# Performance work log

Measured on AMD Instinct MI355X. Metric: run time of the kernel, lower is better.

Reference implementation:

```python
import jax, jax.numpy as jnp
import numpy as np

V, E, H, B, L_ENC, T = 32000, 512, 512, 32, 512, 64


def setup_inputs() -> dict:
    key = jax.random.key(0)
    ks = jax.random.split(key, 15)
    s = 0.05  # weight scale to keep activations in a sane range
    return {
        "x": jax.random.randint(ks[0], (B, 1), 0, V),
        "encod_out": jax.random.normal(ks[1], (B, L_ENC, H), jnp.float32),
        "h": jax.random.normal(ks[2], (1, B, H), jnp.float32) * s,
        "c": jax.random.normal(ks[3], (1, B, H), jnp.float32) * s,
        "targets": jax.random.randint(ks[4], (B, T), 0, V),
        "mask_att": jax.random.randint(ks[5], (B, L_ENC), 0, 2).astype(jnp.int32),
        "teacher_forcing_ratio": 1,
        "embed_table": jax.random.normal(ks[6], (V, E), jnp.float32) * s,
        "W_ih": jax.random.normal(ks[7], (4 * H, E + H), jnp.float32) * s,
        "W_hh": jax.random.normal(ks[8], (4 * H, H), jnp.float32) * s,
        "b_ih": jax.random.normal(ks[9], (4 * H,), jnp.float32) * s,
        "b_hh": jax.random.normal(ks[10], (4 * H,), jnp.float32) * s,
        "W_out": jax.random.normal(ks[11], (V, H), jnp.float32) * s,
        "b_out": jax.random.normal(ks[12], (V,), jnp.float32) * s,
        "mask_logit": jax.random.randint(ks[13], (V,), 0, 2).astype(bool),
    }


def reference(x, encod_out, h, c, targets, mask_att, teacher_forcing_ratio,
              embed_table, W_ih, W_hh, b_ih, b_hh, W_out, b_out, mask_logit):
    # Eval-mode (dropout = identity), teacher forcing ratio = 1.0 (always teacher),
    # num_layers = 1 LSTM. torch LSTM gate order: i, f, g, o.
    neg_inf = jnp.float32(-jnp.inf)
    att_masked = (mask_att == 0)              # (B, L_enc) True -> mask out
    bias = b_ih + b_hh                         # (4H,)
    # Teacher-forced input tokens per step: [x[:,0], targets[:,0..T-2]]
    toks = jnp.concatenate([x[:, :1], targets[:, :-1]], axis=1).T  # (T, B)

    def step(carry, tok):
        hs, cs = carry                          # (B, H) each
        emb = embed_table[tok]                  # (B, E)
        # dot-product attention with last-layer hidden as query
        scores = jnp.einsum('blh,bh->bl', encod_out, hs)      # (B, L_enc)
        scores = jnp.where(att_masked, neg_inf, scores)
        w = jax.nn.softmax(scores, axis=-1)
        ctx = jnp.einsum('bl,blh->bh', w, encod_out)          # (B, H)
        # single-step LSTM cell
        xin = jnp.concatenate([emb, ctx], axis=-1)            # (B, E+H)
        gates = xin @ W_ih.T + hs @ W_hh.T + bias             # (B, 4H)
        i, f, g, o = jnp.split(gates, 4, axis=-1)
        cn = jax.nn.sigmoid(f) * cs + jax.nn.sigmoid(i) * jnp.tanh(g)
        hn = jax.nn.sigmoid(o) * jnp.tanh(cn)
        logit = hn @ W_out.T + b_out                          # (B, V)
        logit = jnp.where(mask_logit, neg_inf, logit)
        return (hn, cn), logit

    (_, _), logits = jax.lax.scan(step, (h[0], c[0]), toks)   # logits: (T, B, V)
    return jnp.transpose(logits, (1, 0, 2))                   # (B, T, V)
```

## Files before the change

kernel.cpp:

```cpp
#include <hip/hip_runtime.h>

#define V_ 32000
#define E_ 512
#define H_ 512
#define B_ 32
#define L_ 512
#define T_ 64
#define G4 2048
#define KX 1024

typedef __attribute__((ext_vector_type(8))) short short8;
typedef __attribute__((ext_vector_type(4))) float f32x4;

#define NEG_INF (-__builtin_inff())
#define MASK_SENTINEL (-1.0e30f)

#define GLOAD_LDS16(g, l)                                                              \
  __builtin_amdgcn_global_load_lds((const __attribute__((address_space(1))) void*)(g), \
                                   (__attribute__((address_space(3))) void*)(l), 16, 0, 0)

__device__ __forceinline__ unsigned short f2bf(float f) {
  unsigned int u = __float_as_uint(f);
  u += 0x7fffu + ((u >> 16) & 1u);
  return (unsigned short)(u >> 16);
}
__device__ __forceinline__ float bf2f(unsigned short u) {
  return __uint_as_float((unsigned int)u << 16);
}
__device__ __forceinline__ float sigmoidf_(float x) { return 1.f / (1.f + expf(-x)); }


__global__ __launch_bounds__(256) void k_cast(const float* __restrict__ W,
                                              unsigned short* __restrict__ Wb) {
  size_t i = ((size_t)blockIdx.x * 256 + threadIdx.x) * 8;
  float4 a = *(const float4*)(W + i);
  float4 b = *(const float4*)(W + i + 4);
  unsigned short r[8] = {f2bf(a.x), f2bf(a.y), f2bf(a.z), f2bf(a.w),
                         f2bf(b.x), f2bf(b.y), f2bf(b.z), f2bf(b.w)};
  *(uint4*)(Wb + i) = *(uint4*)r;
}

__global__ __launch_bounds__(256) void k_pack(const float* __restrict__ Wih, const float* __restrict__ Whh,
                                              const float* __restrict__ bih, const float* __restrict__ bhh,
                                              const float* __restrict__ h0, const float* __restrict__ c0,
                                              unsigned short* __restrict__ WihE, unsigned short* __restrict__ WcH,
                                              float* __restrict__ biasp, float* __restrict__ hf,
                                              float* __restrict__ cf, unsigned short* __restrict__ xin) {
  int bid = blockIdx.x;
  if (bid < G4) {
    int p = bid;
    int j = p >> 5, c = p & 31;
    int ni = c >> 4, g = (c >> 2) & 3, r4 = c & 3;
    int G = g * 512 + j * 8 + ni * 4 + r4;
    for (int k = threadIdx.x; k < KX; k += 256) {
      float w = (k < 512) ? Wih[(size_t)G * 1024 + 512 + k] : Whh[(size_t)G * 512 + (k - 512)];
      WcH[(size_t)p * KX + k] = f2bf(w);
    }
    for (int k = threadIdx.x; k < 512; k += 256)
      WihE[(size_t)p * 512 + k] = f2bf(Wih[(size_t)G * 1024 + k]);
    if (threadIdx.x == 0) biasp[p] = bih[G] + bhh[G];
  } else {
    int b = bid - G4;
    for (int k = threadIdx.x; k < 512; k += 256) {
      float hv = h0[b * 512 + k];
      hf[b * 512 + k] = hv;
      cf[b * 512 + k] = c0[b * 512 + k];
      xin[b * KX + 512 + k] = f2bf(hv);
    }
  }
}

__global__ __launch_bounds__(256) void k_emb(const int* __restrict__ x, const int* __restrict__ targ,
                                             const float* __restrict__ etab, unsigned short* __restrict__ Emb) {
  int m = blockIdx.x;
  int t = m >> 5, b = m & 31;
  int tok = (t == 0) ? x[b] : targ[b * T_ + (t - 1)];
  const float* row = etab + (size_t)tok * E_;
  for (int k = threadIdx.x; k < E_; k += 256)
    Emb[(size_t)m * E_ + k] = f2bf(row[k]);
}

template <int MODE>
__global__ __launch_bounds__(256) void k_gemm128(const unsigned short* __restrict__ A,
                                                 const unsigned short* __restrict__ Bm, int K,
                                                 const float* __restrict__ bias,
                                                 const unsigned char* __restrict__ mask,
                                                 float* __restrict__ C) {
  __shared__ unsigned short As[128 * 32];
  __shared__ unsigned short Bs[128 * 32];
  int tid = threadIdx.x;
  int wave = tid >> 6, lane = tid & 63;
  int wm = wave >> 1, wn = wave & 1;
  int n0 = blockIdx.x * 128, m0 = blockIdx.y * 128;
  int lr = tid >> 2;
  int lc = (tid & 3) * 8;
  int q = lane >> 4, fr = lane & 15;
  f32x4 acc[4][4] = {};
  for (int kk = 0; kk < K; kk += 32) {
    GLOAD_LDS16(&A[(size_t)(m0 + lr) * K + kk + lc],        &As[(wave * 16) * 32]);
    GLOAD_LDS16(&A[(size_t)(m0 + lr + 64) * K + kk + lc],   &As[(wave * 16 + 64) * 32]);
    GLOAD_LDS16(&Bm[(size_t)(n0 + lr) * K + kk + lc],       &Bs[(wave * 16) * 32]);
    GLOAD_LDS16(&Bm[(size_t)(n0 + lr + 64) * K + kk + lc],  &Bs[(wave * 16 + 64) * 32]);
    __syncthreads();
    short8 af[4], bf[4];
#pragma unroll
    for (int i = 0; i < 4; i++) af[i] = *(short8*)&As[(wm * 64 + i * 16 + fr) * 32 + q * 8];
#pragma unroll
    for (int jj = 0; jj < 4; jj++) bf[jj] = *(short8*)&Bs[(wn * 64 + jj * 16 + fr) * 32 + q * 8];
#pragma unroll
    for (int i = 0; i < 4; i++)
#pragma unroll
      for (int jj = 0; jj < 4; jj++)
        acc[i][jj] = __builtin_amdgcn_mfma_f32_16x16x32_bf16(af[i], bf[jj], acc[i][jj], 0, 0, 0);
    __syncthreads();
  }
#pragma unroll
  for (int i = 0; i < 4; i++)
#pragma unroll
    for (int jj = 0; jj < 4; jj++) {
      int col = n0 + wn * 64 + jj * 16 + fr;
#pragma unroll
      for (int e = 0; e < 4; e++) {
        int row = m0 + wm * 64 + i * 16 + q * 4 + e;
        float v = acc[i][jj][e];
        if (MODE == 0) {
          C[(size_t)row * G4 + col] = v + bias[col];
        } else {
          float val = v + bias[col];
          if (mask[col]) val = MASK_SENTINEL;
          int t = row >> 5, b = row & 31;
          C[((size_t)b * T_ + t) * V_ + col] = val;
        }
      }
    }
}

__global__ __launch_bounds__(512) void k_att1(const unsigned short* __restrict__ encb,
                                              const int* __restrict__ matt,
                                              const float* __restrict__ hin,
                                              float* __restrict__ ctxp, float* __restrict__ mS) {
  __shared__ float sc_s[64];
  __shared__ float w_s[64];
  __shared__ float red_s[8 * 512];
  int bid = blockIdx.x;
  int ab = bid >> 3, ach = bid & 7;
  int tid = threadIdx.x, wave = tid >> 6, lane = tid & 63;
  int l0 = ach * 64 + wave * 8;
  float hreg[8];
  {
    const float4* hp = (const float4*)(hin + ab * 512 + lane * 8);
    float4 h0v = hp[0], h1v = hp[1];
    hreg[0] = h0v.x; hreg[1] = h0v.y; hreg[2] = h0v.z; hreg[3] = h0v.w;
    hreg[4] = h1v.x; hreg[5] = h1v.y; hreg[6] = h1v.z; hreg[7] = h1v.w;
  }
  short8 areg[8];
#pragma unroll
  for (int r = 0; r < 8; r++) {
    short8 av = *(const short8*)&encb[((size_t)(ab * L_ + l0 + r)) * H_ + lane * 8];
    areg[r] = av;
    float s = 0.f;
#pragma unroll
    for (int i = 0; i < 8; i++) s += bf2f((unsigned short)av[i]) * hreg[i];
#pragma unroll
    for (int off = 32; off; off >>= 1) s += __shfl_xor(s, off, 64);
    if (matt[ab * L_ + l0 + r] == 0) s = NEG_INF;
    if (lane == 0) sc_s[wave * 8 + r] = s;
  }
  __syncthreads();
  float m = NEG_INF;
#pragma unroll
  for (int i = 0; i < 64; i++) m = fmaxf(m, sc_s[i]);
  float wv[8];
#pragma unroll
  for (int r = 0; r < 8; r++) {
    float s = sc_s[wave * 8 + r];
    wv[r] = (m == NEG_INF) ? 0.f : expf(s - m);
    if (lane == 0) w_s[wave * 8 + r] = wv[r];
  }
  float cpart[8];
#pragma unroll
  for (int i = 0; i < 8; i++) cpart[i] = 0.f;
#pragma unroll
  for (int r = 0; r < 8; r++)
#pragma unroll
    for (int i = 0; i < 8; i++) cpart[i] += wv[r] * bf2f((unsigned short)areg[r][i]);
#pragma unroll
  for (int i = 0; i < 8; i++) red_s[wave * 512 + lane * 8 + i] = cpart[i];
  __syncthreads();
  {
    int jv = tid;
    float s8 = 0.f;
#pragma unroll
    for (int w8 = 0; w8 < 8; w8++) s8 += red_s[w8 * 512 + jv];
    ctxp[(size_t)bid * 512 + jv] = s8;
  }
  if (tid == 0) {
    float S = 0.f;
#pragma unroll
    for (int i = 0; i < 64; i++) S += w_s[i];
    mS[bid * 2] = m;
    mS[bid * 2 + 1] = S;
  }
}

__global__ __launch_bounds__(512) void k_att2(const float* __restrict__ ctxp,
                                              const float* __restrict__ mS,
                                              unsigned short* __restrict__ xin) {
  int b = blockIdx.x, tid = threadIdx.x;
  float m = NEG_INF;
#pragma unroll
  for (int k = 0; k < 8; k++) m = fmaxf(m, mS[(b * 8 + k) * 2]);
  float coef[8];
  float S = 0.f;
#pragma unroll
  for (int k = 0; k < 8; k++) {
    float mk = mS[(b * 8 + k) * 2];
    float ck = (mk == NEG_INF || m == NEG_INF) ? 0.f : expf(mk - m);
    coef[k] = ck;
    S += ck * mS[(b * 8 + k) * 2 + 1];
  }
  float inv = (S > 0.f) ? 1.f / S : 0.f;
  {
    int jv = tid;
    float a = 0.f;
#pragma unroll
    for (int k = 0; k < 8; k++) a += coef[k] * ctxp[((size_t)(b * 8 + k)) * 512 + jv];
    xin[b * KX + jv] = f2bf(a * inv);
  }
}

__global__ __launch_bounds__(256) void k_gates(const unsigned short* __restrict__ xin,
                                               const unsigned short* __restrict__ WcH,
                                               const float* __restrict__ preg, float* __restrict__ hf,
                                               float* __restrict__ cf, unsigned short* __restrict__ xinh,
                                               unsigned short* __restrict__ Hn, int t) {
  __shared__ float g_s[32 * 32];
  int j = blockIdx.x;
  int tid = threadIdx.x, wave = tid >> 6, lane = tid & 63;
  int mi = wave & 1, ni = wave >> 1;
  int q = lane >> 4, fr = lane & 15;
  float pregv[4];
  {
    int c = ni * 16 + fr;
#pragma unroll
    for (int e = 0; e < 4; e++) {
      int brow = mi * 16 + q * 4 + e;
      pregv[e] = preg[((size_t)(t * B_ + brow)) * G4 + j * 32 + c];
    }
  }
  f32x4 acc0 = {}, acc1 = {};
  const unsigned short* Aptr = xin + (size_t)(mi * 16 + fr) * KX + q * 8;
  const unsigned short* Bptr = WcH + (size_t)(j * 32 + ni * 16 + fr) * KX + q * 8;
  for (int kk = 0; kk < KX; kk += 64) {
    short8 af0 = *(const short8*)(Aptr + kk);
    short8 bf0 = *(const short8*)(Bptr + kk);
    short8 af1 = *(const short8*)(Aptr + kk + 32);
    short8 bf1 = *(const short8*)(Bptr + kk + 32);
    acc0 = __builtin_amdgcn_mfma_f32_16x16x32_bf16(af0, bf0, acc0, 0, 0, 0);
    acc1 = __builtin_amdgcn_mfma_f32_16x16x32_bf16(af1, bf1, acc1, 0, 0, 0);
  }
#pragma unroll
  for (int e = 0; e < 4; e++) {
    int brow = mi * 16 + q * 4 + e;
    int c = ni * 16 + fr;
    g_s[brow * 32 + c] = acc0[e] + acc1[e] + pregv[e];
  }
  __syncthreads();
  int b = tid >> 3, r = tid & 7;
  int ni2 = r >> 2, r4 = r & 3;
  float iv = g_s[b * 32 + ni2 * 16 + 0 * 4 + r4];
  float fv = g_s[b * 32 + ni2 * 16 + 1 * 4 + r4];
  float gv = g_s[b * 32 + ni2 * 16 + 2 * 4 + r4];
  float ov = g_s[b * 32 + ni2 * 16 + 3 * 4 + r4];
  int hcol = j * 8 + r;
  float cold = cf[b * 512 + hcol];
  float cn = sigmoidf_(fv) * cold + sigmoidf_(iv) * tanhf(gv);
  float hn = sigmoidf_(ov) * tanhf(cn);
  cf[b * 512 + hcol] = cn;
  hf[b * 512 + hcol] = hn;
  unsigned short hb = f2bf(hn);
  xinh[b * KX + 512 + hcol] = hb;
  Hn[((size_t)(t * B_ + b)) * H_ + hcol] = hb;
}


extern "C" void kernel_launch(void* const* d_in, const int* in_sizes, int n_in, void* d_out,
                              int out_size, void* d_ws, size_t ws_size, hipStream_t stream) {
  const int* x = (const int*)d_in[0];
  const float* enc = (const float*)d_in[1];
  const float* h0 = (const float*)d_in[2];
  const float* c0 = (const float*)d_in[3];
  const int* targ = (const int*)d_in[4];
  const int* matt = (const int*)d_in[5];
  const float* etab = (const float*)d_in[7];
  const float* Wih = (const float*)d_in[8];
  const float* Whh = (const float*)d_in[9];
  const float* bih = (const float*)d_in[10];
  const float* bhh = (const float*)d_in[11];
  const float* Wout = (const float*)d_in[12];
  const float* bout = (const float*)d_in[13];
  const unsigned char* mlog = (const unsigned char*)d_in[14];
  float* out = (float*)d_out;

  char* ws = (char*)d_ws;
  size_t o = 0;
  unsigned short* Woutb = (unsigned short*)(ws + o); o += (size_t)V_ * H_ * 2;
  unsigned short* encb  = (unsigned short*)(ws + o); o += (size_t)B_ * L_ * H_ * 2;
  unsigned short* Emb   = (unsigned short*)(ws + o); o += (size_t)T_ * B_ * E_ * 2;
  unsigned short* WihE  = (unsigned short*)(ws + o); o += (size_t)G4 * E_ * 2;
  unsigned short* WcH   = (unsigned short*)(ws + o); o += (size_t)G4 * KX * 2;
  float* preg           = (float*)(ws + o);          o += (size_t)T_ * B_ * G4 * 4;
  float* biasp          = (float*)(ws + o);          o += (size_t)G4 * 4;
  float* hf             = (float*)(ws + o);          o += (size_t)B_ * H_ * 4;
  float* cf             = (float*)(ws + o);          o += (size_t)B_ * H_ * 4;
  unsigned short* xin   = (unsigned short*)(ws + o); o += (size_t)B_ * KX * 2;
  float* ctxp           = (float*)(ws + o);          o += (size_t)B_ * 8 * H_ * 4;
  float* mS             = (float*)(ws + o);          o += (size_t)B_ * 8 * 2 * 4;
  unsigned short* Hn    = (unsigned short*)(ws + o); o += (size_t)T_ * B_ * H_ * 2;

  hipLaunchKernelGGL(k_cast, dim3((V_ * H_) / (256 * 8)), dim3(256), 0, stream, Wout, Woutb);
  hipLaunchKernelGGL(k_cast, dim3((B_ * L_ * H_) / (256 * 8)), dim3(256), 0, stream, enc, encb);
  hipLaunchKernelGGL(k_pack, dim3(G4 + B_), dim3(256), 0, stream, Wih, Whh, bih, bhh, h0, c0, WihE,
                     WcH, biasp, hf, cf, xin);
  hipLaunchKernelGGL(k_emb, dim3(T_ * B_), dim3(256), 0, stream, x, targ, etab, Emb);
  hipLaunchKernelGGL((k_gemm128<0>), dim3(G4 / 128, (T_ * B_) / 128), dim3(256), 0, stream, Emb,
                     WihE, E_, biasp, (const unsigned char*)nullptr, preg);

  for (int t = 0; t < T_; t++) {
    hipLaunchKernelGGL(k_att1, dim3(B_ * 8), dim3(512), 0, stream, encb, matt, hf, ctxp, mS);
    hipLaunchKernelGGL(k_att2, dim3(B_), dim3(512), 0, stream, ctxp, mS, xin);
    hipLaunchKernelGGL(k_gates, dim3(64), dim3(256), 0, stream, xin, WcH, preg, hf, cf, xin, Hn, t);
  }

  hipLaunchKernelGGL((k_gemm128<1>), dim3(V_ / 128, (T_ * B_) / 128), dim3(256), 0, stream, Hn,
                     Woutb, H_, bout, mlog, out);
}
```

Baseline: 1.891 ms.

## Fuse attention score and context kernels into one per-batch online-softmax kernel

Merges the two attention kernels into one kernel that runs one block per batch row. Each wave streams 64 encoder rows with an online softmax and the waves are combined in shared memory. This removes a kernel launch per step and the global partial-context buffer. In exchange, block-level parallelism drops from 256 to 32 blocks for a bandwidth-bound read of the encoder.

```diff
diff --git a/kernel.cpp b/kernel.cpp
--- a/kernel.cpp
+++ b/kernel.cpp
@@ -135,96 +135,80 @@
     }
 }
 
-__global__ __launch_bounds__(512) void k_att1(const unsigned short* __restrict__ encb,
-                                              const int* __restrict__ matt,
-                                              const float* __restrict__ hin,
-                                              float* __restrict__ ctxp, float* __restrict__ mS) {
-  __shared__ float sc_s[64];
-  __shared__ float w_s[64];
+__global__ __launch_bounds__(512) void k_att(const unsigned short* __restrict__ encb,
+                                             const int* __restrict__ matt,
+                                             const float* __restrict__ hin,
+                                             unsigned short* __restrict__ xin) {
   __shared__ float red_s[8 * 512];
-  int bid = blockIdx.x;
-  int ab = bid >> 3, ach = bid & 7;
+  __shared__ float mS_s[8][2];
+  int b = blockIdx.x;
   int tid = threadIdx.x, wave = tid >> 6, lane = tid & 63;
-  int l0 = ach * 64 + wave * 8;
   float hreg[8];
   {
-    const float4* hp = (const float4*)(hin + ab * 512 + lane * 8);
+    const float4* hp = (const float4*)(hin + b * 512 + lane * 8);
     float4 h0v = hp[0], h1v = hp[1];
     hreg[0] = h0v.x; hreg[1] = h0v.y; hreg[2] = h0v.z; hreg[3] = h0v.w;
     hreg[4] = h1v.x; hreg[5] = h1v.y; hreg[6] = h1v.z; hreg[7] = h1v.w;
   }
-  short8 areg[8];
-#pragma unroll
-  for (int r = 0; r < 8; r++) {
-    short8 av = *(const short8*)&encb[((size_t)(ab * L_ + l0 + r)) * H_ + lane * 8];
-    areg[r] = av;
-    float s = 0.f;
-#pragma unroll
-    for (int i = 0; i < 8; i++) s += bf2f((unsigned short)av[i]) * hreg[i];
-#pragma unroll
-    for (int off = 32; off; off >>= 1) s += __shfl_xor(s, off, 64);
-    if (matt[ab * L_ + l0 + r] == 0) s = NEG_INF;
-    if (lane == 0) sc_s[wave * 8 + r] = s;
-  }
+  float cpart[8] = {0.f, 0.f, 0.f, 0.f, 0.f, 0.f, 0.f, 0.f};
+  float mw = NEG_INF, Sw = 0.f;
+  for (int rep = 0; rep < 8; ++rep) {
+    int l0 = wave * 64 + rep * 8;
+    short8 areg[8];
+    float sc[8];
+#pragma unroll
+    for (int r = 0; r < 8; r++) {
+      short8 av = *(const short8*)&encb[((size_t)(b * L_ + l0 + r)) * H_ + lane * 8];
+      areg[r] = av;
+      float s = 0.f;
+#pragma unroll
+      for (int i = 0; i < 8; i++) s += bf2f((unsigned short)av[i]) * hreg[i];
+#pragma unroll
+      for (int off = 32; off; off >>= 1) s += __shfl_xor(s, off, 64);
+      if (matt[b * L_ + l0 + r] == 0) s = NEG_INF;
+      sc[r] = s;
+    }
+    float rmax = sc[0];
+#pragma unroll
+    for (int r = 1; r < 8; r++) rmax = fmaxf(rmax, sc[r]);
+    if (rmax != NEG_INF) {
+      float mnew = fmaxf(mw, rmax);
+      float scale = expf(mw - mnew);
+      Sw *= scale;
+#pragma unroll
+      for (int i = 0; i < 8; i++) cpart[i] *= scale;
+      mw = mnew;
+#pragma unroll
+      for (int r = 0; r < 8; r++) {
+        float wv = expf(sc[r] - mw);
+        Sw += wv;
+#pragma unroll
+        for (int i = 0; i < 8; i++) cpart[i] += wv * bf2f((unsigned short)areg[r][i]);
+      }
+    }
+  }
+  if (lane == 0) { mS_s[wave][0] = mw; mS_s[wave][1] = Sw; }
   __syncthreads();
   float m = NEG_INF;
 #pragma unroll
-  for (int i = 0; i < 64; i++) m = fmaxf(m, sc_s[i]);
-  float wv[8];
-#pragma unroll
-  for (int r = 0; r < 8; r++) {
-    float s = sc_s[wave * 8 + r];
-    wv[r] = (m == NEG_INF) ? 0.f : expf(s - m);
-    if (lane == 0) w_s[wave * 8 + r] = wv[r];
-  }
-  float cpart[8];
-#pragma unroll
-  for (int i = 0; i < 8; i++) cpart[i] = 0.f;
-#pragma unroll
-  for (int r = 0; r < 8; r++)
-#pragma unroll
-    for (int i = 0; i < 8; i++) cpart[i] += wv[r] * bf2f((unsigned short)areg[r][i]);
-#pragma unroll
-  for (int i = 0; i < 8; i++) red_s[wave * 512 + lane * 8 + i] = cpart[i];
+  for (int w = 0; w < 8; w++) m = fmaxf(m, mS_s[w][0]);
+  float S = 0.f;
+#pragma unroll
+  for (int w = 0; w < 8; w++) {
+    float mk = mS_s[w][0];
+    float ck = (mk == NEG_INF || m == NEG_INF) ? 0.f : expf(mk - m);
+    S += ck * mS_s[w][1];
+  }
+  float coefw = (mw == NEG_INF || m == NEG_INF) ? 0.f : expf(mw - m);
+#pragma unroll
+  for (int i = 0; i < 8; i++) red_s[wave * 512 + lane * 8 + i] = coefw * cpart[i];
   __syncthreads();
-  {
-    int jv = tid;
-    float s8 = 0.f;
-#pragma unroll
-    for (int w8 = 0; w8 < 8; w8++) s8 += red_s[w8 * 512 + jv];
-    ctxp[(size_t)bid * 512 + jv] = s8;
-  }
-  if (tid == 0) {
-    float S = 0.f;
-#pragma unroll
-    for (int i = 0; i < 64; i++) S += w_s[i];
-    mS[bid * 2] = m;
-    mS[bid * 2 + 1] = S;
-  }
-}
-
-__global__ __launch_bounds__(512) void k_att2(const float* __restrict__ ctxp,
-                                              const float* __restrict__ mS,
-                                              unsigned short* __restrict__ xin) {
-  int b = blockIdx.x, tid = threadIdx.x;
-  float m = NEG_INF;
-#pragma unroll
-  for (int k = 0; k < 8; k++) m = fmaxf(m, mS[(b * 8 + k) * 2]);
-  float coef[8];
-  float S = 0.f;
-#pragma unroll
-  for (int k = 0; k < 8; k++) {
-    float mk = mS[(b * 8 + k) * 2];
-    float ck = (mk == NEG_INF || m == NEG_INF) ? 0.f : expf(mk - m);
-    coef[k] = ck;
-    S += ck * mS[(b * 8 + k) * 2 + 1];
-  }
   float inv = (S > 0.f) ? 1.f / S : 0.f;
   {
     int jv = tid;
     float a = 0.f;
 #pragma unroll
-    for (int k = 0; k < 8; k++) a += coef[k] * ctxp[((size_t)(b * 8 + k)) * 512 + jv];
+    for (int w = 0; w < 8; w++) a += red_s[w * 512 + jv];
     xin[b * KX + jv] = f2bf(a * inv);
   }
 }
@@ -314,8 +298,6 @@
   float* hf             = (float*)(ws + o);          o += (size_t)B_ * H_ * 4;
   float* cf             = (float*)(ws + o);          o += (size_t)B_ * H_ * 4;
   unsigned short* xin   = (unsigned short*)(ws + o); o += (size_t)B_ * KX * 2;
-  float* ctxp           = (float*)(ws + o);          o += (size_t)B_ * 8 * H_ * 4;
-  float* mS             = (float*)(ws + o);          o += (size_t)B_ * 8 * 2 * 4;
   unsigned short* Hn    = (unsigned short*)(ws + o); o += (size_t)T_ * B_ * H_ * 2;
 
   hipLaunchKernelGGL(k_cast, dim3((V_ * H_) / (256 * 8)), dim3(256), 0, stream, Wout, Woutb);
@@ -327,8 +309,7 @@
                      WihE, E_, biasp, (const unsigned char*)nullptr, preg);
 
   for (int t = 0; t < T_; t++) {
-    hipLaunchKernelGGL(k_att1, dim3(B_ * 8), dim3(512), 0, stream, encb, matt, hf, ctxp, mS);
-    hipLaunchKernelGGL(k_att2, dim3(B_), dim3(512), 0, stream, ctxp, mS, xin);
+    hipLaunchKernelGGL(k_att, dim3(B_), dim3(512), 0, stream, encb, matt, hf, xin);
     hipLaunchKernelGGL(k_gates, dim3(64), dim3(256), 0, stream, xin, WcH, preg, hf, cf, xin, Hn, t);
   }
 
```

New measurement: 2.236 ms. 18.2% more time.
